# Kernel tuning notes

Measured on AMD Instinct MI355X. Metric: run time of the kernel, lower is better.

## Reference

```python
import jax, jax.numpy as jnp
from jax import lax
import numpy as np

B = 128      # graphs
L = 128      # nodes (tokens) per graph
N = B * L    # total nodes
E = 262144   # edges (avg degree 16)
VOCAB = 50000
EMB = 300
H = 256      # lstm hidden per direction
GCN = 512
NCLS = 2
EPS = 1e-12


def lstm_dir(x, wih, whh, b, reverse):
    # x: [B, L, EMB]; wih: [4H, EMB]; whh: [4H, H]; b: [4H]
    bsz, seq, _ = x.shape
    hdim = whh.shape[1]
    xs = jnp.einsum('ble,ge->blg', x, wih) + b  # [B, L, 4H]
    if reverse:
        xs = xs[:, ::-1]
    def step(carry, xt):
        h, c = carry
        gates = xt + h @ whh.T
        i, f, g, o = jnp.split(gates, 4, axis=-1)  # torch gate order i,f,g,o
        i = jax.nn.sigmoid(i); f = jax.nn.sigmoid(f)
        g = jnp.tanh(g); o = jax.nn.sigmoid(o)
        c = f * c + i * g
        h = o * jnp.tanh(c)
        return (h, c), h
    h0 = jnp.zeros((bsz, hdim), x.dtype)
    _, hs = lax.scan(step, (h0, h0), jnp.swapaxes(xs, 0, 1))
    hs = jnp.swapaxes(hs, 0, 1)  # [B, L, H]
    if reverse:
        hs = hs[:, ::-1]
    return hs


def sage_conv(x, src, dst, Wl, bl, Wr):
    # PyG SAGEConv(mean, normalize=True): lin_l(mean_j x_j) + lin_r(x_i), then L2-normalize
    msg = x[src]                                              # [E, d] gather
    agg = jax.ops.segment_sum(msg, dst, num_segments=x.shape[0])
    cnt = jax.ops.segment_sum(jnp.ones((src.shape[0], 1), x.dtype), dst,
                              num_segments=x.shape[0])
    agg = agg / jnp.maximum(cnt, 1.0)
    out = agg @ Wl + bl + x @ Wr
    nrm = jnp.linalg.norm(out, axis=-1, keepdims=True)
    return out / jnp.maximum(nrm, EPS)


def setup_inputs() -> dict:
    key = jax.random.key(0)
    ks = jax.random.split(key, 24)
    word_seq = jax.random.randint(ks[0], (B, L), 0, VOCAB)
    # intra-graph edges: local endpoints + graph offset
    el = jax.random.randint(ks[1], (2, E), 0, L)
    gid = jnp.repeat(jnp.arange(E // (E // B) * 0 + B), E // B)  # [E]
    edge_index = el + gid[None, :] * L
    batch = jnp.repeat(jnp.arange(B), L)
    s = 0.05
    inp = {
        'word_seq': word_seq, 'edge_index': edge_index, 'batch': batch,
        'embed_table': jax.random.normal(ks[2], (VOCAB, EMB), jnp.float32) * 0.1,
        'wih_f': jax.random.normal(ks[3], (4 * H, EMB), jnp.float32) * s,
        'whh_f': jax.random.normal(ks[4], (4 * H, H), jnp.float32) * s,
        'b_f': jax.random.normal(ks[5], (4 * H,), jnp.float32) * s,
        'wih_b': jax.random.normal(ks[6], (4 * H, EMB), jnp.float32) * s,
        'whh_b': jax.random.normal(ks[7], (4 * H, H), jnp.float32) * s,
        'b_b': jax.random.normal(ks[8], (4 * H,), jnp.float32) * s,
        'Wl1': jax.random.normal(ks[9], (2 * H, GCN), jnp.float32) * s,
        'Wr1': jax.random.normal(ks[10], (2 * H, GCN), jnp.float32) * s,
        'b1': jnp.zeros((GCN,), jnp.float32),
        'Wl2': jax.random.normal(ks[11], (GCN, 512), jnp.float32) * s,
        'Wr2': jax.random.normal(ks[12], (GCN, 512), jnp.float32) * s,
        'b2': jnp.zeros((512,), jnp.float32),
        'Wl3': jax.random.normal(ks[13], (512, 512), jnp.float32) * s,
        'Wr3': jax.random.normal(ks[14], (512, 512), jnp.float32) * s,
        'b3': jnp.zeros((512,), jnp.float32),
        'Wlin': jax.random.normal(ks[15], (512, NCLS), jnp.float32) * s,
        'blin': jnp.zeros((NCLS,), jnp.float32),
    }
    return inp


def reference(word_seq, edge_index, batch, embed_table,
              wih_f, whh_f, b_f, wih_b, whh_b, b_b,
              Wl1, Wr1, b1, Wl2, Wr2, b2, Wl3, Wr3, b3, Wlin, blin):
    # embedding (frozen) over padded per-graph sequences; uniform lengths -> plain reshape
    xe = embed_table[word_seq]                       # [B, L, EMB]
    hf = lstm_dir(xe, wih_f, whh_f, b_f, reverse=False)
    hb = lstm_dir(xe, wih_b, whh_b, b_b, reverse=True)
    x = jnp.concatenate([hf, hb], axis=-1).reshape(N, 2 * H)  # node features
    src, dst = edge_index[0], edge_index[1]
    x = jax.nn.relu(sage_conv(x, src, dst, Wl1, b1, Wr1))
    x = jax.nn.relu(sage_conv(x, src, dst, Wl2, b2, Wr2))
    x = jax.nn.relu(sage_conv(x, src, dst, Wl3, b3, Wr3))
    # global mean pool over graphs
    s = jax.ops.segment_sum(x, batch, num_segments=B)
    c = jax.ops.segment_sum(jnp.ones((N, 1), x.dtype), batch, num_segments=B)
    pooled = s / jnp.maximum(c, 1.0)
    return pooled @ Wlin + blin                      # [B, NCLS]
```

## Files before the change

### kernel.cpp

```cpp
#include <hip/hip_runtime.h>
#include <math.h>

#define NN   16384
#define EE   262144

typedef __attribute__((ext_vector_type(8))) short  short8v;
typedef __attribute__((ext_vector_type(4))) float  f32x4;

__device__ inline unsigned short f2bf(float f) {
    union { float f; unsigned u; } v; v.f = f;
    unsigned r = v.u + 0x7fff + ((v.u >> 16) & 1);
    return (unsigned short)(r >> 16);
}
__device__ inline float bf2f(unsigned short b) {
    unsigned u = ((unsigned)b) << 16;
    union { unsigned u; float f; } v; v.u = u; return v.f;
}
__device__ inline float sigm_f(float x) { return 1.f / (1.f + __expf(-x)); }
__device__ inline float tanh_f(float x) {
    x = fminf(15.f, fmaxf(-15.f, x));
    float e = __expf(2.f * x);
    return (e - 1.f) / (e + 1.f);
}
__device__ inline int gate_orig2(int np) {
    int Q = np >> 8, wv = (np >> 5) & 7, tile = (np >> 4) & 1, tc = np & 15;
    int g = tile * 2 + (tc >> 3);
    int j = Q * 64 + wv * 8 + (tc & 7);
    return g * 256 + j;
}

__global__ void k_init(unsigned long long* __restrict__ hx, int* __restrict__ deg,
                       int* __restrict__ fill) {
    int i = blockIdx.x * 256 + threadIdx.x;
    if (i < 65536) hx[i] = 0ull;
    if (i < NN) { deg[i] = 0; fill[i] = 0; }
}

__global__ void k_embed_bf(const int* __restrict__ wseq, const float* __restrict__ tab,
                           unsigned short* __restrict__ xeb) {
    int i = blockIdx.x * 256 + threadIdx.x;
    if (i >= NN * 320) return;
    int row = i / 320, k = i - row * 320;
    float f = (k < 300) ? tab[wseq[row] * 300 + k] : 0.f;
    xeb[i] = f2bf(f);
}

__global__ void k_cvt_wih(const float* __restrict__ wih, unsigned short* __restrict__ wt) {
    int i = blockIdx.x * 256 + threadIdx.x;
    if (i >= 1024 * 320) return;
    int np = i / 320, k = i - np * 320;
    wt[i] = f2bf(k < 300 ? wih[gate_orig2(np) * 300 + k] : 0.f);
}
__global__ void k_cvt_whh(const float* __restrict__ whh, unsigned short* __restrict__ wp) {
    int i = blockIdx.x * 256 + threadIdx.x;
    if (i >= 1024 * 256) return;
    int np = i >> 8, k = i & 255;
    wp[i] = f2bf(whh[gate_orig2(np) * 256 + k]);
}
__global__ void k_permb(const float* __restrict__ b, float* __restrict__ pb) {
    int i = blockIdx.x * 256 + threadIdx.x;
    if (i < 1024) pb[i] = b[gate_orig2(i)];
}
__global__ void k_cvt_wcat(const float* __restrict__ Wl, const float* __restrict__ Wr,
                           unsigned short* __restrict__ wc) {
    int i = blockIdx.x * 256 + threadIdx.x;
    if (i >= 512 * 1024) return;
    int n = i >> 10, k = i & 1023;
    float f = (k < 512) ? Wl[k * 512 + n] : Wr[(k - 512) * 512 + n];
    wc[i] = f2bf(f);
}

__global__ __launch_bounds__(256)
void k_mgemm(const unsigned short* __restrict__ A, const unsigned short* __restrict__ Bt,
             const float* __restrict__ bias, float* __restrict__ C, int N, int Ka)
{
    __shared__ unsigned short As[128 * 32];
    __shared__ unsigned short Bs[128 * 32];
    const int tid = threadIdx.x;
    const int m0 = blockIdx.x << 7, n0 = blockIdx.y << 7;
    const int w = tid >> 6, lane = tid & 63;
    const int wr = w >> 1, wc = w & 1;
    const int lr = lane & 15, lhi = lane >> 4;
    const int r0 = tid >> 2, kc0 = (tid & 3) * 8;

    f32x4 acc[4][4] = {};

    for (int k0 = 0; k0 < Ka; k0 += 32) {
        short8v a0 = *(const short8v*)(A + (m0 + r0) * Ka + k0 + kc0);
        short8v a1 = *(const short8v*)(A + (m0 + 64 + r0) * Ka + k0 + kc0);
        short8v b0 = *(const short8v*)(Bt + (n0 + r0) * Ka + k0 + kc0);
        short8v b1 = *(const short8v*)(Bt + (n0 + 64 + r0) * Ka + k0 + kc0);
        __syncthreads();
        *(short8v*)&As[r0 * 32 + kc0]        = a0;
        *(short8v*)&As[(64 + r0) * 32 + kc0] = a1;
        *(short8v*)&Bs[r0 * 32 + kc0]        = b0;
        *(short8v*)&Bs[(64 + r0) * 32 + kc0] = b1;
        __syncthreads();
        short8v af[4], bf[4];
        #pragma unroll
        for (int i = 0; i < 4; ++i)
            af[i] = *(const short8v*)&As[(wr * 64 + i * 16 + lr) * 32 + lhi * 8];
        #pragma unroll
        for (int j = 0; j < 4; ++j)
            bf[j] = *(const short8v*)&Bs[(wc * 64 + j * 16 + lr) * 32 + lhi * 8];
        #pragma unroll
        for (int i = 0; i < 4; ++i)
            #pragma unroll
            for (int j = 0; j < 4; ++j)
                acc[i][j] = __builtin_amdgcn_mfma_f32_16x16x32_bf16(af[i], bf[j], acc[i][j], 0, 0, 0);
    }
    #pragma unroll
    for (int i = 0; i < 4; ++i) {
        int row = m0 + wr * 64 + i * 16 + lhi * 4;
        #pragma unroll
        for (int j = 0; j < 4; ++j) {
            int col = n0 + wc * 64 + j * 16 + lr;
            float bv = bias[col];
            #pragma unroll
            for (int r = 0; r < 4; ++r)
                C[(row + r) * N + col] = acc[i][j][r] + bv;
        }
    }
}

__global__ __launch_bounds__(512, 2)
void k_lstm(const float* __restrict__ xs_f, const float* __restrict__ xs_b,
            const unsigned short* __restrict__ whhp_f, const unsigned short* __restrict__ whhp_b,
            unsigned short* __restrict__ xout, unsigned long long* __restrict__ hx)
{
    const int tid  = threadIdx.x;
    const int wv   = tid >> 6, lane = tid & 63;
    const int lr16 = lane & 15, lh = lane >> 4;
    const int b3   = (lane >> 3) & 1, lr3 = lane & 7;
    const int wgid = blockIdx.x;
    const int dir  = wgid >> 5;
    const int bs   = (wgid >> 2) & 7;
    const int Q    = wgid & 3;
    const int b0   = bs * 16;
    const float* xs = dir ? xs_b : xs_f;
    const unsigned short* whhp = dir ? whhp_b : whhp_f;

    const int ncol0 = Q * 256 + wv * 32 + lr16;
    short8v wf[2][8];
    #pragma unroll
    for (int tt = 0; tt < 2; ++tt)
        #pragma unroll
        for (int ks = 0; ks < 8; ++ks)
            wf[tt][ks] = *(const short8v*)(whhp
                + (size_t)(ncol0 + tt * 16) * 256 + ks * 32 + lh * 8);

    __shared__ unsigned short At[2][16 * 256];

    const int grpbase = (dir * 8 + bs) * 4 * 1024;
    unsigned long long* hx_own = hx + grpbase + Q * 1024;

    const int jmine = Q * 64 + wv * 8 + lr3;
    const int rowb  = 4 * lh;
    const int myr0  = rowb + 2 * b3;
    const int up_jl = (tid >> 6) * 8 + (tid & 7);
    const int up_r0 = 2 * ((tid >> 3) & 7);

    float c0 = 0.f, c1 = 0.f;
    float xv0[4], xv1[4];
    {
        const int l0 = dir ? 127 : 0;
        #pragma unroll
        for (int r = 0; r < 4; ++r) {
            const float* xp = xs + ((size_t)(b0 + rowb + r) * 128 + l0) * 1024;
            xv0[r] = xp[ncol0];
            xv1[r] = xp[ncol0 + 16];
        }
    }

    for (int t = 0; t < 128; ++t) {
        const int l = dir ? (127 - t) : t;
        f32x4 acc0 = {}, acc1 = {};
        if (t > 0) {
            const char* Ab = (const char*)&At[(t - 1) & 1][0];
            #pragma unroll
            for (int ks = 0; ks < 8; ++ks) {
                int off = (lr16 * 512 + ks * 64 + lh * 16) ^ ((lr16 & 7) << 4);
                short8v a = *(const short8v*)(Ab + off);
                acc0 = __builtin_amdgcn_mfma_f32_16x16x32_bf16(a, wf[0][ks], acc0, 0, 0, 0);
                acc1 = __builtin_amdgcn_mfma_f32_16x16x32_bf16(a, wf[1][ks], acc1, 0, 0, 0);
            }
        }
        #pragma unroll
        for (int r = 0; r < 4; ++r) { acc0[r] += xv0[r]; acc1[r] += xv1[r]; }
        float z0 = b3 ? acc0[0] : acc0[2];
        float z1 = b3 ? acc0[1] : acc0[3];
        float z2 = b3 ? acc1[0] : acc1[2];
        float z3 = b3 ? acc1[1] : acc1[3];
        float y0 = __shfl_xor(z0, 8);
        float y1 = __shfl_xor(z1, 8);
        float y2 = __shfl_xor(z2, 8);
        float y3 = __shfl_xor(z3, 8);
        float iv0 = b3 ? y0 : acc0[0], iv1 = b3 ? y1 : acc0[1];
        float fv0 = b3 ? acc0[2] : y0, fv1 = b3 ? acc0[3] : y1;
        float gv0 = b3 ? y2 : acc1[0], gv1 = b3 ? y3 : acc1[1];
        float ov0 = b3 ? acc1[2] : y2, ov1 = b3 ? acc1[3] : y3;
        iv0 = sigm_f(iv0); fv0 = sigm_f(fv0); gv0 = tanh_f(gv0); ov0 = sigm_f(ov0);
        c0 = fv0 * c0 + iv0 * gv0;
        float h0 = ov0 * tanh_f(c0);
        iv1 = sigm_f(iv1); fv1 = sigm_f(fv1); gv1 = tanh_f(gv1); ov1 = sigm_f(ov1);
        c1 = fv1 * c1 + iv1 * gv1;
        float h1 = ov1 * tanh_f(c1);
        unsigned short hb0 = f2bf(h0), hb1 = f2bf(h1);
        xout[((size_t)(b0 + myr0)     * 128 + l) * 512 + dir * 256 + jmine] = hb0;
        xout[((size_t)(b0 + myr0 + 1) * 128 + l) * 512 + dir * 256 + jmine] = hb1;

        if (t < 127) {
            const int p = t & 1;
            char* Aw = (char*)&At[p][0];
            {
                int r0_ = myr0, r1_ = myr0 + 1;
                *(unsigned short*)(Aw + ((r0_ * 512 + 2 * jmine) ^ ((r0_ & 7) << 4))) = hb0;
                *(unsigned short*)(Aw + ((r1_ * 512 + 2 * jmine) ^ ((r1_ & 7) << 4))) = hb1;
            }
            const unsigned tg = (unsigned)(t + 1);
            unsigned long long w = ((unsigned long long)tg << 32)
                                 | ((unsigned)hb0 | ((unsigned)hb1 << 16));
            __hip_atomic_store(hx_own + p * 512 + tid, w,
                               __ATOMIC_RELAXED, __HIP_MEMORY_SCOPE_AGENT);
            const int l2 = dir ? (126 - t) : (t + 1);
            #pragma unroll
            for (int r = 0; r < 4; ++r) {
                const float* xp = xs + ((size_t)(b0 + rowb + r) * 128 + l2) * 1024;
                xv0[r] = xp[ncol0];
                xv1[r] = xp[ncol0 + 16];
            }
            const unsigned long long* pp1 = hx + grpbase + (Q ^ 1) * 1024 + p * 512 + tid;
            const unsigned long long* pp2 = hx + grpbase + (Q ^ 2) * 1024 + p * 512 + tid;
            const unsigned long long* pp3 = hx + grpbase + (Q ^ 3) * 1024 + p * 512 + tid;
            unsigned long long u1 = __hip_atomic_load(pp1, __ATOMIC_RELAXED, __HIP_MEMORY_SCOPE_AGENT);
            unsigned long long u2 = __hip_atomic_load(pp2, __ATOMIC_RELAXED, __HIP_MEMORY_SCOPE_AGENT);
            unsigned long long u3 = __hip_atomic_load(pp3, __ATOMIC_RELAXED, __HIP_MEMORY_SCOPE_AGENT);
            while ((unsigned)(u1 >> 32) != tg)
                u1 = __hip_atomic_load(pp1, __ATOMIC_RELAXED, __HIP_MEMORY_SCOPE_AGENT);
            while ((unsigned)(u2 >> 32) != tg)
                u2 = __hip_atomic_load(pp2, __ATOMIC_RELAXED, __HIP_MEMORY_SCOPE_AGENT);
            while ((unsigned)(u3 >> 32) != tg)
                u3 = __hip_atomic_load(pp3, __ATOMIC_RELAXED, __HIP_MEMORY_SCOPE_AGENT);
            {
                int ra = up_r0, rb = up_r0 + 1;
                int j1 = (Q ^ 1) * 64 + up_jl;
                int j2 = (Q ^ 2) * 64 + up_jl;
                int j3 = (Q ^ 3) * 64 + up_jl;
                *(unsigned short*)(Aw + ((ra * 512 + 2 * j1) ^ ((ra & 7) << 4))) =
                    (unsigned short)(u1 & 0xffff);
                *(unsigned short*)(Aw + ((rb * 512 + 2 * j1) ^ ((rb & 7) << 4))) =
                    (unsigned short)((u1 >> 16) & 0xffff);
                *(unsigned short*)(Aw + ((ra * 512 + 2 * j2) ^ ((ra & 7) << 4))) =
                    (unsigned short)(u2 & 0xffff);
                *(unsigned short*)(Aw + ((rb * 512 + 2 * j2) ^ ((rb & 7) << 4))) =
                    (unsigned short)((u2 >> 16) & 0xffff);
                *(unsigned short*)(Aw + ((ra * 512 + 2 * j3) ^ ((ra & 7) << 4))) =
                    (unsigned short)(u3 & 0xffff);
                *(unsigned short*)(Aw + ((rb * 512 + 2 * j3) ^ ((rb & 7) << 4))) =
                    (unsigned short)((u3 >> 16) & 0xffff);
            }
            __syncthreads();
        }
    }
}

__global__ void k_hist(const int* __restrict__ ei, int* __restrict__ deg) {
    int e = blockIdx.x * 256 + threadIdx.x;
    if (e >= EE) return;
    atomicAdd(&deg[ei[EE + e]], 1);
}

__global__ void k_scan(const int* __restrict__ deg, int* __restrict__ indptr) {
    __shared__ int sm[256];
    int tid = threadIdx.x;
    int b0 = tid * 64;
    int s = 0;
    for (int i = 0; i < 64; ++i) s += deg[b0 + i];
    sm[tid] = s;
    __syncthreads();
    for (int off = 1; off < 256; off <<= 1) {
        int v = (tid >= off) ? sm[tid - off] : 0;
        __syncthreads();
        sm[tid] += v;
        __syncthreads();
    }
    int run = sm[tid] - s;
    for (int i = 0; i < 64; ++i) { indptr[b0 + i] = run; run += deg[b0 + i]; }
    if (tid == 255) indptr[NN] = run;
}

__global__ void k_scatter(const int* __restrict__ ei, const int* __restrict__ indptr,
                          int* __restrict__ fill, int* __restrict__ cols) {
    int e = blockIdx.x * 256 + threadIdx.x;
    if (e >= EE) return;
    int d = ei[EE + e];
    int slot = atomicAdd(&fill[d], 1);
    cols[indptr[d] + slot] = ei[e];
}

__global__ __launch_bounds__(256)
void k_gather_bf(const unsigned short* __restrict__ x, const int* __restrict__ indptr,
                 const int* __restrict__ cols, unsigned short* __restrict__ catb)
{
    int gw = (blockIdx.x * 256 + threadIdx.x) >> 6;
    int lane = threadIdx.x & 63;
    if (gw >= NN) return;
    int s = indptr[gw], e = indptr[gw + 1];
    float a[8] = {};
    for (int p = s; p < e; ++p) {
        short8v v = *(const short8v*)(x + cols[p] * 512 + lane * 8);
        #pragma unroll
        for (int q = 0; q < 8; ++q) a[q] += bf2f((unsigned short)v[q]);
    }
    float sc = 1.f / (float)((e - s) > 1 ? (e - s) : 1);
    unsigned short* cp = catb + gw * 1024 + lane * 8;
    unsigned short o[8];
    #pragma unroll
    for (int q = 0; q < 8; ++q) o[q] = f2bf(a[q] * sc);
    *(short8v*)cp = *(short8v*)o;
    *(short8v*)(cp + 512) = *(const short8v*)(x + gw * 512 + lane * 8);
}

__global__ __launch_bounds__(256)
void k_norm_relu_bf(const float* __restrict__ y, unsigned short* __restrict__ o)
{
    int gw = (blockIdx.x * 256 + threadIdx.x) >> 6;
    int lane = threadIdx.x & 63;
    if (gw >= NN) return;
    const float* row = y + gw * 512 + lane * 8;
    float4 v0 = *(const float4*)row;
    float4 v1 = *(const float4*)(row + 4);
    float ss = v0.x*v0.x + v0.y*v0.y + v0.z*v0.z + v0.w*v0.w
             + v1.x*v1.x + v1.y*v1.y + v1.z*v1.z + v1.w*v1.w;
    #pragma unroll
    for (int off = 32; off >= 1; off >>= 1) ss += __shfl_xor(ss, off);
    float sc = 1.f / fmaxf(sqrtf(ss), 1e-12f);
    unsigned short ob[8];
    ob[0] = f2bf(fmaxf(v0.x*sc, 0.f)); ob[1] = f2bf(fmaxf(v0.y*sc, 0.f));
    ob[2] = f2bf(fmaxf(v0.z*sc, 0.f)); ob[3] = f2bf(fmaxf(v0.w*sc, 0.f));
    ob[4] = f2bf(fmaxf(v1.x*sc, 0.f)); ob[5] = f2bf(fmaxf(v1.y*sc, 0.f));
    ob[6] = f2bf(fmaxf(v1.z*sc, 0.f)); ob[7] = f2bf(fmaxf(v1.w*sc, 0.f));
    *(short8v*)(o + gw * 512 + lane * 8) = *(short8v*)ob;
}

__global__ __launch_bounds__(256)
void k_pool_bf(const unsigned short* __restrict__ x, const float* __restrict__ Wlin,
               const float* __restrict__ blin, float* __restrict__ out)
{
    int g = blockIdx.x;
    int tid = threadIdx.x;
    const unsigned short* base = x + (size_t)g * 128 * 512;
    float a0 = 0.f, a1 = 0.f;
    for (int r = 0; r < 128; ++r) {
        unsigned v = *(const unsigned*)(base + r * 512 + 2 * tid);
        a0 += bf2f((unsigned short)(v & 0xffff));
        a1 += bf2f((unsigned short)(v >> 16));
    }
    __shared__ float pooled[512];
    pooled[2*tid]     = a0 * (1.f / 128.f);
    pooled[2*tid + 1] = a1 * (1.f / 128.f);
    __syncthreads();
    if (tid < 64) {
        float p0 = 0.f, p1 = 0.f;
        for (int k = tid; k < 512; k += 64) {
            float pv = pooled[k];
            p0 += pv * Wlin[2*k];
            p1 += pv * Wlin[2*k + 1];
        }
        #pragma unroll
        for (int off = 32; off >= 1; off >>= 1) {
            p0 += __shfl_xor(p0, off);
            p1 += __shfl_xor(p1, off);
        }
        if (tid == 0) {
            out[2*g]     = p0 + blin[0];
            out[2*g + 1] = p1 + blin[1];
        }
    }
}

extern "C" void kernel_launch(void* const* d_in, const int* in_sizes, int n_in,
                              void* d_out, int out_size, void* d_ws, size_t ws_size,
                              hipStream_t stream)
{
    (void)in_sizes; (void)n_in; (void)out_size; (void)ws_size;
    const int*   word_seq = (const int*)  d_in[0];
    const int*   ei       = (const int*)  d_in[1];
    const float* tab      = (const float*)d_in[3];
    const float* wih_f    = (const float*)d_in[4];
    const float* whh_f    = (const float*)d_in[5];
    const float* b_f      = (const float*)d_in[6];
    const float* wih_b    = (const float*)d_in[7];
    const float* whh_b    = (const float*)d_in[8];
    const float* b_b      = (const float*)d_in[9];
    const float* Wl1      = (const float*)d_in[10];
    const float* Wr1      = (const float*)d_in[11];
    const float* b1       = (const float*)d_in[12];
    const float* Wl2      = (const float*)d_in[13];
    const float* Wr2      = (const float*)d_in[14];
    const float* b2       = (const float*)d_in[15];
    const float* Wl3      = (const float*)d_in[16];
    const float* Wr3      = (const float*)d_in[17];
    const float* b3       = (const float*)d_in[18];
    const float* Wlin     = (const float*)d_in[19];
    const float* blin     = (const float*)d_in[20];
    float* out = (float*)d_out;

    char* w = (char*)d_ws;
    int*   deg    = (int*)  (w);
    int*   indptr = (int*)  (w + 65536);
    int*   fill   = (int*)  (w + 131584);
    int*   cols   = (int*)  (w + 197120);
    unsigned long long* hx = (unsigned long long*)(w + 1245696);
    unsigned short* whhp_f = (unsigned short*)(w + 1769984);
    unsigned short* whhp_b = (unsigned short*)(w + 2294272);
    float* pb_f   = (float*)(w + 2818560);
    float* pb_b   = (float*)(w + 2822656);
    unsigned short* wt_f = (unsigned short*)(w + 2826752);
    unsigned short* wt_b = (unsigned short*)(w + 3482112);
    unsigned short* wc1  = (unsigned short*)(w + 4137472);
    unsigned short* wc2  = (unsigned short*)(w + 5186048);
    unsigned short* wc3  = (unsigned short*)(w + 6234624);
    unsigned short* xeb  = (unsigned short*)(w + 7283200);
    float* xs_f   = (float*)(w + 17768960);
    float* xs_b   = (float*)(w + 84877824);
    unsigned short* x0b = (unsigned short*)(w + 151986688);
    unsigned short* catb = (unsigned short*)(w + 17768960);
    float* x1     = (float*)(w + 51323392);
    unsigned short* xb_a = (unsigned short*)(w + 84877824);
    unsigned short* xb_b = (unsigned short*)(w + 101655040);

    k_embed_bf<<<20480, 256, 0, stream>>>(word_seq, tab, xeb);
    k_cvt_wih<<<1280, 256, 0, stream>>>(wih_f, wt_f);
    k_cvt_wih<<<1280, 256, 0, stream>>>(wih_b, wt_b);
    k_cvt_whh<<<1024, 256, 0, stream>>>(whh_f, whhp_f);
    k_cvt_whh<<<1024, 256, 0, stream>>>(whh_b, whhp_b);
    k_permb<<<4, 256, 0, stream>>>(b_f, pb_f);
    k_permb<<<4, 256, 0, stream>>>(b_b, pb_b);
    k_cvt_wcat<<<2048, 256, 0, stream>>>(Wl1, Wr1, wc1);
    k_cvt_wcat<<<2048, 256, 0, stream>>>(Wl2, Wr2, wc2);
    k_cvt_wcat<<<2048, 256, 0, stream>>>(Wl3, Wr3, wc3);

    k_init<<<256, 256, 0, stream>>>(hx, deg, fill);
    k_hist<<<1024, 256, 0, stream>>>(ei, deg);
    k_scan<<<1, 256, 0, stream>>>(deg, indptr);
    k_scatter<<<1024, 256, 0, stream>>>(ei, indptr, fill, cols);

    k_mgemm<<<dim3(128, 8), 256, 0, stream>>>(xeb, wt_f, pb_f, xs_f, 1024, 320);
    k_mgemm<<<dim3(128, 8), 256, 0, stream>>>(xeb, wt_b, pb_b, xs_b, 1024, 320);

    k_lstm<<<64, 512, 0, stream>>>(xs_f, xs_b, whhp_f, whhp_b, x0b, hx);

    k_gather_bf<<<4096, 256, 0, stream>>>(x0b, indptr, cols, catb);
    k_mgemm<<<dim3(128, 4), 256, 0, stream>>>(catb, wc1, b1, x1, 512, 1024);
    k_norm_relu_bf<<<4096, 256, 0, stream>>>(x1, xb_a);
    k_gather_bf<<<4096, 256, 0, stream>>>(xb_a, indptr, cols, catb);
    k_mgemm<<<dim3(128, 4), 256, 0, stream>>>(catb, wc2, b2, x1, 512, 1024);
    k_norm_relu_bf<<<4096, 256, 0, stream>>>(x1, xb_b);
    k_gather_bf<<<4096, 256, 0, stream>>>(xb_b, indptr, cols, catb);
    k_mgemm<<<dim3(128, 4), 256, 0, stream>>>(catb, wc3, b3, x1, 512, 1024);
    k_norm_relu_bf<<<4096, 256, 0, stream>>>(x1, xb_a);

    k_pool_bf<<<128, 256, 0, stream>>>(xb_a, Wlin, blin, out);
}
```

Measured before the change: 653.3 us.

## Stage each graph's node features in LDS for SAGE neighbor gather

Replaces the per-node global-memory neighbor gather with a kernel that loads a whole graph's 128x512 bf16 feature block (128 KB) into LDS, then aggregates neighbors from LDS. Two blocks per graph each handle 64 nodes. This relies on edges being intra-graph, which the input construction guarantees. It cuts the scattered global or L2 reads, but each graph block is loaded twice and the 128 KB dynamic LDS limits occupancy to one block per CU, with only 256 blocks in total.

```diff
diff --git a/kernel.cpp b/kernel.cpp
--- a/kernel.cpp
+++ b/kernel.cpp
@@ -298,27 +298,45 @@
     cols[indptr[d] + slot] = ei[e];
 }
 
-__global__ __launch_bounds__(256)
-void k_gather_bf(const unsigned short* __restrict__ x, const int* __restrict__ indptr,
-                 const int* __restrict__ cols, unsigned short* __restrict__ catb)
-{
-    int gw = (blockIdx.x * 256 + threadIdx.x) >> 6;
-    int lane = threadIdx.x & 63;
-    if (gw >= NN) return;
-    int s = indptr[gw], e = indptr[gw + 1];
-    float a[8] = {};
-    for (int p = s; p < e; ++p) {
-        short8v v = *(const short8v*)(x + cols[p] * 512 + lane * 8);
-        #pragma unroll
-        for (int q = 0; q < 8; ++q) a[q] += bf2f((unsigned short)v[q]);
-    }
-    float sc = 1.f / (float)((e - s) > 1 ? (e - s) : 1);
-    unsigned short* cp = catb + gw * 1024 + lane * 8;
-    unsigned short o[8];
-    #pragma unroll
-    for (int q = 0; q < 8; ++q) o[q] = f2bf(a[q] * sc);
-    *(short8v*)cp = *(short8v*)o;
-    *(short8v*)(cp + 512) = *(const short8v*)(x + gw * 512 + lane * 8);
+__global__ __launch_bounds__(512)
+void k_gather_lds(const unsigned short* __restrict__ x, const int* __restrict__ indptr,
+                  const int* __restrict__ cols, unsigned short* __restrict__ catb)
+{
+    extern __shared__ char gsm[];
+    unsigned short* Xs = (unsigned short*)gsm;
+    const int tid  = threadIdx.x;
+    const int g    = blockIdx.x >> 1;
+    const int hf   = blockIdx.x & 1;
+    const int base = g * 128;
+    {
+        const unsigned short* src = x + (size_t)base * 512;
+        #pragma unroll
+        for (int it = 0; it < 16; ++it) {
+            int i = it * 512 + tid;
+            int row = i >> 6, c = (i & 63) * 8;
+            *(short8v*)(Xs + row * 512 + c) = *(const short8v*)(src + (size_t)row * 512 + c);
+        }
+    }
+    __syncthreads();
+    const int wv = tid >> 6, lane = tid & 63;
+    for (int rr = 0; rr < 8; ++rr) {
+        int node = base + hf * 64 + rr * 8 + wv;
+        int s = indptr[node], e = indptr[node + 1];
+        float a[8] = {};
+        for (int p = s; p < e; ++p) {
+            int lrow = cols[p] - base;
+            short8v v = *(const short8v*)(Xs + lrow * 512 + lane * 8);
+            #pragma unroll
+            for (int q = 0; q < 8; ++q) a[q] += bf2f((unsigned short)v[q]);
+        }
+        float sc = 1.f / (float)((e - s) > 1 ? (e - s) : 1);
+        unsigned short o[8];
+        #pragma unroll
+        for (int q = 0; q < 8; ++q) o[q] = f2bf(a[q] * sc);
+        unsigned short* cp = catb + (size_t)node * 1024 + lane * 8;
+        *(short8v*)cp = *(short8v*)o;
+        *(short8v*)(cp + 512) = *(const short8v*)(Xs + (node - base) * 512 + lane * 8);
+    }
 }
 
 __global__ __launch_bounds__(256)
@@ -451,13 +469,13 @@
 
     k_lstm<<<64, 512, 0, stream>>>(xs_f, xs_b, whhp_f, whhp_b, x0b, hx);
 
-    k_gather_bf<<<4096, 256, 0, stream>>>(x0b, indptr, cols, catb);
+    k_gather_lds<<<256, 512, 131072, stream>>>(x0b, indptr, cols, catb);
     k_mgemm<<<dim3(128, 4), 256, 0, stream>>>(catb, wc1, b1, x1, 512, 1024);
     k_norm_relu_bf<<<4096, 256, 0, stream>>>(x1, xb_a);
-    k_gather_bf<<<4096, 256, 0, stream>>>(xb_a, indptr, cols, catb);
+    k_gather_lds<<<256, 512, 131072, stream>>>(xb_a, indptr, cols, catb);
     k_mgemm<<<dim3(128, 4), 256, 0, stream>>>(catb, wc2, b2, x1, 512, 1024);
     k_norm_relu_bf<<<4096, 256, 0, stream>>>(x1, xb_b);
-    k_gather_bf<<<4096, 256, 0, stream>>>(xb_b, indptr, cols, catb);
+    k_gather_lds<<<256, 512, 131072, stream>>>(xb_b, indptr, cols, catb);
     k_mgemm<<<dim3(128, 4), 256, 0, stream>>>(catb, wc3, b3, x1, 512, 1024);
     k_norm_relu_bf<<<4096, 256, 0, stream>>>(x1, xb_a);
 
```

Result: no change. 646.5 us (-1.0%).
